# Performance work log

Measured on AMD Instinct MI355X. Metric: run time of the kernel, lower is better.

Reference implementation:

```python
import jax, jax.numpy as jnp
import numpy as np

N_NODES = 8192
N_EDGES = 524288
IN_DIM = 256
HID1 = 128
HID2 = 64


def setup_inputs() -> dict:
    key = jax.random.key(0)
    ks = jax.random.split(key, 10)
    s = 0.05
    x = jax.random.normal(ks[0], (N_NODES, IN_DIM), dtype=jnp.float32)
    edge_index = jax.random.randint(ks[1], (2, N_EDGES), 0, N_NODES, dtype=jnp.int64)
    W1 = jax.random.normal(ks[2], (IN_DIM, HID1), dtype=jnp.float32) * s
    b1 = jnp.zeros((HID1,), dtype=jnp.float32)
    W2 = jax.random.normal(ks[3], (IN_DIM, HID1), dtype=jnp.float32) * s
    b2 = jnp.zeros((HID1,), dtype=jnp.float32)
    Wmu = jax.random.normal(ks[4], (2 * HID1, HID2), dtype=jnp.float32) * s
    bmu = jnp.zeros((HID2,), dtype=jnp.float32)
    Wlv = jax.random.normal(ks[5], (2 * HID1, HID2), dtype=jnp.float32) * s
    blv = jnp.zeros((HID2,), dtype=jnp.float32)
    return {"x": x, "edge_index": edge_index, "W1": W1, "b1": b1,
            "W2": W2, "b2": b2, "Wmu": Wmu, "bmu": bmu, "Wlv": Wlv, "blv": blv}


def _gcn(x, W, b, row, col, norm, n):
    # linear transform, edge-indexed gather, degree-normalized scale, scatter-add
    h = x @ W                                   # [N, out]
    msg = h[col] * norm[:, None]                # [E+N, out]
    agg = jax.ops.segment_sum(msg, row, num_segments=n)
    return agg + b


def reference(x, edge_index, W1, b1, W2, b2, Wmu, bmu, Wlv, blv):
    n = x.shape[0]
    loop = jnp.arange(n, dtype=edge_index.dtype)
    row = jnp.concatenate([edge_index[0], loop])   # add self-loops (GCNConv default)
    col = jnp.concatenate([edge_index[1], loop])
    deg = jax.ops.segment_sum(jnp.ones_like(row, dtype=x.dtype), row, num_segments=n)
    dinv = jnp.where(deg > 0, jax.lax.rsqrt(deg), 0.0)
    norm = dinv[row] * dinv[col]                   # symmetric D^-1/2 A_hat D^-1/2

    h1 = _gcn(x, W1, b1, row, col, norm, n)
    h2 = _gcn(x, W2, b2, row, col, norm, n)
    hc = jnp.concatenate([h1, h2], axis=1)         # [N, 2*HID1]
    mu = _gcn(hc, Wmu, bmu, row, col, norm, n)
    logvar = _gcn(hc, Wlv, blv, row, col, norm, n)
    z = mu                                         # eval-mode reparametrize -> mu
    adj = jax.nn.sigmoid(z @ z.T)                  # InnerProductDecoder.forward_all
    return adj, mu, logvar
```

## Files before the change

### kernel.cpp

```cpp
#include <hip/hip_runtime.h>
#include <hip/hip_bf16.h>

#define N_NODES 8192
#define N_EDGES 524288
#define TOT_EDGES (N_EDGES + N_NODES)
#define IN_DIM 256
#define HID1 128
#define HID2 64
#define DC 128
#define CAP 192
#define FILL_BLK 520

typedef __attribute__((ext_vector_type(8))) short bf16x8;
typedef __attribute__((ext_vector_type(4))) float f32x4;
typedef __attribute__((ext_vector_type(4))) int   i32x4;
typedef __attribute__((ext_vector_type(4))) unsigned short u16x4;

__device__ __forceinline__ float b2f(unsigned short u){
    unsigned int v = ((unsigned int)u) << 16;
    float f; __builtin_memcpy(&f, &v, 4); return f;
}
__device__ __forceinline__ unsigned short f2b(float f){
    __hip_bfloat16 h = __float2bfloat16(f);
    return *(unsigned short*)&h;
}


__global__ __launch_bounds__(256) void k_pre(const float* __restrict__ x, unsigned short* __restrict__ xbf,
                                             const float* __restrict__ W1, const float* __restrict__ W2,
                                             const float* __restrict__ Wmu, const float* __restrict__ Wlv,
                                             const float* __restrict__ b1, const float* __restrict__ b2,
                                             unsigned short* __restrict__ WcT, float* __restrict__ cvec,
                                             float* __restrict__ zbase){
    int b = blockIdx.x, t = threadIdx.x;
    if (b < 2048){
        int g = (b*256 + t)*4;
        f32x4 v = *(const f32x4*)(x + g);
        u16x4 o;
        #pragma unroll
        for (int j=0;j<4;j++) o[j] = f2b(v[j]);
        *(u16x4*)(xbf + g) = o;
    } else if (b < 2176){
        int r = (b - 2048)*2 + (t >> 7);
        int j = t & 127;
        const float* Wsel = (j < 64) ? Wmu : Wlv;
        int jj = j & 63;
        float acc = 0.f;
        for (int k=0;k<HID1;k++){
            acc += W1[r*HID1+k] * Wsel[k*HID2+jj] + W2[r*HID1+k] * Wsel[(HID1+k)*HID2+jj];
        }
        WcT[(size_t)j*IN_DIM + r] = f2b(acc);
        if (r == 0){
            float c = 0.f;
            for (int k=0;k<HID1;k++){
                c += b1[k]*Wsel[k*HID2+jj] + b2[k]*Wsel[(HID1+k)*HID2+jj];
            }
            cvec[j] = c;
        }
    } else {
        ((f32x4*)zbase)[(b-2176)*256 + t] = (f32x4){0.f,0.f,0.f,0.f};
    }
}


__global__ __launch_bounds__(256) void k_fill_gemm(const int* __restrict__ ei, int* __restrict__ fillc,
                                                   unsigned short* __restrict__ slots,
                                                   const unsigned short* __restrict__ xbf,
                                                   const unsigned short* __restrict__ WcT,
                                                   unsigned short* __restrict__ Ubf){
    int b = blockIdx.x, t = threadIdx.x;
    if (b < FILL_BLK){
        int e4 = (b*256 + t)*4;
        if (e4 >= TOT_EDGES) return;
        if (e4 < N_EDGES){
            i32x4 rr = *(const i32x4*)(ei + e4);
            i32x4 cc = *(const i32x4*)(ei + N_EDGES + e4);
            #pragma unroll
            for (int j=0;j<4;j++){
                int s = atomicAdd(&fillc[rr[j]], 1);
                if (s < CAP) slots[(size_t)rr[j]*CAP + s] = (unsigned short)cc[j];
            }
        } else {
            #pragma unroll
            for (int j=0;j<4;j++){
                int r = e4 - N_EDGES + j;
                int s = atomicAdd(&fillc[r], 1);
                if (s < CAP) slots[(size_t)r*CAP + s] = (unsigned short)r;
            }
        }
    } else {
        int l  = t & 63;
        int w  = t >> 6;
        int Ibase = (b - FILL_BLK)*32;
        int Jbase = w*32;
        int lr = l & 15;
        int kg = l >> 4;
        f32x4 acc[2][2];
        #pragma unroll
        for (int mt=0;mt<2;mt++)
            #pragma unroll
            for (int nt=0;nt<2;nt++) acc[mt][nt] = (f32x4){0.f,0.f,0.f,0.f};
        #pragma unroll
        for (int kc=0; kc<IN_DIM/32; kc++){
            bf16x8 a[2], bb[2];
            #pragma unroll
            for (int mt=0;mt<2;mt++)
                a[mt] = *(const bf16x8*)(xbf + (size_t)(Ibase+mt*16+lr)*IN_DIM + kc*32 + kg*8);
            #pragma unroll
            for (int nt=0;nt<2;nt++)
                bb[nt] = *(const bf16x8*)(WcT + (size_t)(Jbase+nt*16+lr)*IN_DIM + kc*32 + kg*8);
            #pragma unroll
            for (int mt=0;mt<2;mt++)
                #pragma unroll
                for (int nt=0;nt<2;nt++)
                    acc[mt][nt] = __builtin_amdgcn_mfma_f32_16x16x32_bf16(a[mt], bb[nt], acc[mt][nt], 0, 0, 0);
        }
        #pragma unroll
        for (int mt=0;mt<2;mt++)
            #pragma unroll
            for (int r=0;r<4;r++){
                int grow = Ibase + mt*16 + kg*4 + r;
                #pragma unroll
                for (int nt=0;nt<2;nt++)
                    Ubf[(size_t)grow*DC + Jbase + nt*16 + lr] = f2b(acc[mt][nt][r]);
            }
    }
}


__global__ __launch_bounds__(256) void k_spmm(const unsigned short* __restrict__ IN,
                                              const unsigned short* __restrict__ slots,
                                              const int* __restrict__ fillc,
                                              unsigned short* __restrict__ OUT){
    int tid = threadIdx.x;
    int i = blockIdx.x*4 + (tid >> 6);
    int l  = tid & 15;
    int eg = (tid >> 4) & 3;
    int deg = min(fillc[i], CAP);
    const unsigned short* sl = slots + (size_t)i*CAP;
    float acc[8] = {0.f,0.f,0.f,0.f,0.f,0.f,0.f,0.f};
    for (int e = eg; e < deg; e += 4){
        int c = sl[e];
        float wgt = rsqrtf((float)fillc[c]);
        bf16x8 v = *(const bf16x8*)(IN + (size_t)c*DC + l*8);
        #pragma unroll
        for (int j=0;j<8;j++) acc[j] += wgt * b2f((unsigned short)v[j]);
    }
    #pragma unroll
    for (int j=0;j<8;j++){
        acc[j] += __shfl_xor(acc[j], 16);
        acc[j] += __shfl_xor(acc[j], 32);
    }
    if (eg == 0){
        float di = rsqrtf((float)fillc[i]);
        bf16x8 o;
        #pragma unroll
        for (int j=0;j<8;j++) o[j] = (short)f2b(di*acc[j]);
        *(bf16x8*)(OUT + (size_t)i*DC + l*8) = o;
    }
}


__global__ __launch_bounds__(256) void k_spmm_out(const unsigned short* __restrict__ T,
                                                  const unsigned short* __restrict__ slots,
                                                  const int* __restrict__ fillc,
                                                  const float* __restrict__ cvec,
                                                  const float* __restrict__ bmu, const float* __restrict__ blv,
                                                  float* __restrict__ outMu, float* __restrict__ outLv,
                                                  unsigned short* __restrict__ muBf){
    int tid = threadIdx.x;
    int i = blockIdx.x*4 + (tid >> 6);
    int l  = tid & 15;
    int eg = (tid >> 4) & 3;
    int deg = min(fillc[i], CAP);
    const unsigned short* sl = slots + (size_t)i*CAP;
    float acc[8] = {0.f,0.f,0.f,0.f,0.f,0.f,0.f,0.f};
    float wsum = 0.f;
    for (int e = eg; e < deg; e += 4){
        int c = sl[e];
        float wgt = rsqrtf((float)fillc[c]);
        wsum += wgt;
        bf16x8 v = *(const bf16x8*)(T + (size_t)c*DC + l*8);
        #pragma unroll
        for (int j=0;j<8;j++) acc[j] += wgt * b2f((unsigned short)v[j]);
    }
    #pragma unroll
    for (int j=0;j<8;j++){
        acc[j] += __shfl_xor(acc[j], 16);
        acc[j] += __shfl_xor(acc[j], 32);
    }
    wsum += __shfl_xor(wsum, 16);
    wsum += __shfl_xor(wsum, 32);
    if (eg == 0){
        float di = rsqrtf((float)fillc[i]);
        float sv = di * wsum;
        float val[8];
        #pragma unroll
        for (int j=0;j<8;j++) val[j] = di*acc[j] + sv*cvec[l*8+j];
        if (l < 8){
            f32x4 v0, v1; bf16x8 o;
            #pragma unroll
            for (int j=0;j<8;j++){
                float vv = val[j] + bmu[l*8+j];
                if (j<4) v0[j] = vv; else v1[j-4] = vv;
                o[j] = (short)f2b(vv);
            }
            *(f32x4*)(outMu + (size_t)i*HID2 + l*8)     = v0;
            *(f32x4*)(outMu + (size_t)i*HID2 + l*8 + 4) = v1;
            *(bf16x8*)(muBf + (size_t)i*HID2 + l*8)     = o;
        } else {
            int d = (l-8)*8;
            f32x4 v0, v1;
            #pragma unroll
            for (int j=0;j<8;j++){
                float vv = val[j] + blv[d+j];
                if (j<4) v0[j] = vv; else v1[j-4] = vv;
            }
            *(f32x4*)(outLv + (size_t)i*HID2 + d)     = v0;
            *(f32x4*)(outLv + (size_t)i*HID2 + d + 4) = v1;
        }
    }
}


__global__ __launch_bounds__(256) void k_adj(const unsigned short* __restrict__ mu, float* __restrict__ adj){
    int t  = threadIdx.x;
    int l  = t & 63;
    int w  = t >> 6;
    int wr = w >> 1, wc = w & 1;
    int Ibase = blockIdx.y*128 + wr*64;
    int Jbase0 = blockIdx.x*128;
    int Jbase = Jbase0 + wc*64;
    int lr = l & 15;
    int kg = l >> 4;

    bf16x8 afr[4][2], bfr[4][2];
    #pragma unroll
    for (int mt=0; mt<4; mt++){
        const unsigned short* p = mu + (size_t)(Ibase + mt*16 + lr)*HID2 + kg*8;
        afr[mt][0] = *(const bf16x8*)(p);
        afr[mt][1] = *(const bf16x8*)(p + 32);
    }
    #pragma unroll
    for (int nt=0; nt<4; nt++){
        const unsigned short* p = mu + (size_t)(Jbase + nt*16 + lr)*HID2 + kg*8;
        bfr[nt][0] = *(const bf16x8*)(p);
        bfr[nt][1] = *(const bf16x8*)(p + 32);
    }

    f32x4 acc[4][4];
    #pragma unroll
    for (int mt=0; mt<4; mt++)
        #pragma unroll
        for (int nt=0; nt<4; nt++)
            acc[mt][nt] = (f32x4){0.f,0.f,0.f,0.f};

    #pragma unroll
    for (int kc=0; kc<2; kc++)
        #pragma unroll
        for (int mt=0; mt<4; mt++)
            #pragma unroll
            for (int nt=0; nt<4; nt++)
                acc[mt][nt] = __builtin_amdgcn_mfma_f32_16x16x32_bf16(afr[mt][kc], bfr[nt][kc], acc[mt][nt], 0, 0, 0);

    __shared__ float tile[64][132];
    int rowBlockBase = blockIdx.y*128;
    #pragma unroll
    for (int p=0; p<2; p++){
        if (wr == p){
            #pragma unroll
            for (int mt=0; mt<4; mt++)
                #pragma unroll
                for (int r=0; r<4; r++){
                    int row_local = mt*16 + kg*4 + r;
                    #pragma unroll
                    for (int nt=0; nt<4; nt++)
                        tile[row_local][wc*64 + nt*16 + lr] = acc[mt][nt][r];
                }
        }
        __syncthreads();
        #pragma unroll
        for (int rep=0; rep<8; rep++){
            int row_r = rep*8 + (t >> 5);
            int col   = (t & 31)*4;
            f32x4 v = *(const f32x4*)&tile[row_r][col];
            f32x4 o;
            #pragma unroll
            for (int j=0;j<4;j++)
                o[j] = __builtin_amdgcn_rcpf(1.f + __expf(-v[j]));
            int grow = rowBlockBase + p*64 + row_r;
            *(f32x4*)(adj + (size_t)grow*N_NODES + Jbase0 + col) = o;
        }
        __syncthreads();
    }
}


extern "C" void kernel_launch(void* const* d_in, const int* in_sizes, int n_in,
                              void* d_out, int out_size, void* d_ws, size_t ws_size,
                              hipStream_t stream){
    const float* x   = (const float*)d_in[0];
    const int*   ei  = (const int*)  d_in[1];
    const float* W1  = (const float*)d_in[2];
    const float* b1  = (const float*)d_in[3];
    const float* W2  = (const float*)d_in[4];
    const float* b2  = (const float*)d_in[5];
    const float* Wmu = (const float*)d_in[6];
    const float* bmu = (const float*)d_in[7];
    const float* Wlv = (const float*)d_in[8];
    const float* blv = (const float*)d_in[9];

    char* ws = (char*)d_ws;
    int*   fillc  = (int*)  (ws + 0);
    unsigned short* WcT = (unsigned short*)(ws + 32768);
    float* cvec   = (float*)(ws + 98304);
    unsigned short* muBf = (unsigned short*)(ws + 98816);
    unsigned short* xbf  = (unsigned short*)(ws + 1147392);

    float* adj   = (float*)d_out;
    float* outMu = adj + (size_t)N_NODES*N_NODES;
    float* outLv = outMu + (size_t)N_NODES*HID2;

    unsigned short* Ubf   = (unsigned short*)adj;
    unsigned short* Tbf   = (unsigned short*)((char*)adj + 16*1024*1024);
    unsigned short* slots = (unsigned short*)((char*)adj + 32*1024*1024);

    k_pre      <<<2184, 256, 0, stream>>>(x, xbf, W1, W2, Wmu, Wlv, b1, b2, WcT, cvec, (float*)ws);
    k_fill_gemm<<<FILL_BLK + 256, 256, 0, stream>>>(ei, fillc, slots, xbf, WcT, Ubf);
    k_spmm     <<<N_NODES/4, 256, 0, stream>>>(Ubf, slots, fillc, Tbf);
    k_spmm_out <<<N_NODES/4, 256, 0, stream>>>(Tbf, slots, fillc, cvec, bmu, blv,
                                               outMu, outLv, muBf);
    k_adj      <<<dim3(N_NODES/128, N_NODES/128), 256, 0, stream>>>(muBf, adj);
}
```

Before: 133.0 us.

## Fuse x bf16 conversion into GEMM and use per-wave adj epilogue

Drops the separate pass that converts x to bf16 in k_pre; the GEMM now loads fp32 x directly and converts in registers, which removes an 8 MB read plus a 4 MB write and makes k_pre much smaller. The adj epilogue switches from a block-wide shared tile with __syncthreads to a per-wave 16x64 LDS staging buffer that uses only waitcnt, so no block barriers are needed and less shared memory is used. In exchange, each GEMM block now reads twice as many bytes of x, and the adj row stores become narrower (256B per row segment rather than 512B).

```diff
diff --git a/kernel.cpp b/kernel.cpp
--- a/kernel.cpp
+++ b/kernel.cpp
@@ -26,22 +26,16 @@
 }
 
 
-__global__ __launch_bounds__(256) void k_pre(const float* __restrict__ x, unsigned short* __restrict__ xbf,
-                                             const float* __restrict__ W1, const float* __restrict__ W2,
+__global__ __launch_bounds__(256) void k_pre(const float* __restrict__ W1, const float* __restrict__ W2,
                                              const float* __restrict__ Wmu, const float* __restrict__ Wlv,
                                              const float* __restrict__ b1, const float* __restrict__ b2,
                                              unsigned short* __restrict__ WcT, float* __restrict__ cvec,
                                              float* __restrict__ zbase){
     int b = blockIdx.x, t = threadIdx.x;
-    if (b < 2048){
-        int g = (b*256 + t)*4;
-        f32x4 v = *(const f32x4*)(x + g);
-        u16x4 o;
-        #pragma unroll
-        for (int j=0;j<4;j++) o[j] = f2b(v[j]);
-        *(u16x4*)(xbf + g) = o;
-    } else if (b < 2176){
-        int r = (b - 2048)*2 + (t >> 7);
+    if (b < 8){
+        ((f32x4*)zbase)[b*256 + t] = (f32x4){0.f,0.f,0.f,0.f};
+    } else {
+        int r = (b - 8)*2 + (t >> 7);
         int j = t & 127;
         const float* Wsel = (j < 64) ? Wmu : Wlv;
         int jj = j & 63;
@@ -57,15 +51,13 @@
             }
             cvec[j] = c;
         }
-    } else {
-        ((f32x4*)zbase)[(b-2176)*256 + t] = (f32x4){0.f,0.f,0.f,0.f};
     }
 }
 
 
 __global__ __launch_bounds__(256) void k_fill_gemm(const int* __restrict__ ei, int* __restrict__ fillc,
                                                    unsigned short* __restrict__ slots,
-                                                   const unsigned short* __restrict__ xbf,
+                                                   const float* __restrict__ x,
                                                    const unsigned short* __restrict__ WcT,
                                                    unsigned short* __restrict__ Ubf){
     int b = blockIdx.x, t = threadIdx.x;
@@ -104,8 +96,16 @@
         for (int kc=0; kc<IN_DIM/32; kc++){
             bf16x8 a[2], bb[2];
             #pragma unroll
-            for (int mt=0;mt<2;mt++)
-                a[mt] = *(const bf16x8*)(xbf + (size_t)(Ibase+mt*16+lr)*IN_DIM + kc*32 + kg*8);
+            for (int mt=0;mt<2;mt++){
+                const float* xr = x + (size_t)(Ibase+mt*16+lr)*IN_DIM + kc*32 + kg*8;
+                f32x4 v0 = *(const f32x4*)xr;
+                f32x4 v1 = *(const f32x4*)(xr + 4);
+                #pragma unroll
+                for (int j=0;j<4;j++){
+                    a[mt][j]   = (short)f2b(v0[j]);
+                    a[mt][4+j] = (short)f2b(v1[j]);
+                }
+            }
             #pragma unroll
             for (int nt=0;nt<2;nt++)
                 bb[nt] = *(const bf16x8*)(WcT + (size_t)(Jbase+nt*16+lr)*IN_DIM + kc*32 + kg*8);
@@ -229,8 +229,7 @@
     int w  = t >> 6;
     int wr = w >> 1, wc = w & 1;
     int Ibase = blockIdx.y*128 + wr*64;
-    int Jbase0 = blockIdx.x*128;
-    int Jbase = Jbase0 + wc*64;
+    int Jbase = blockIdx.x*128 + wc*64;
     int lr = l & 15;
     int kg = l >> 4;
 
@@ -263,35 +262,29 @@
             for (int nt=0; nt<4; nt++)
                 acc[mt][nt] = __builtin_amdgcn_mfma_f32_16x16x32_bf16(afr[mt][kc], bfr[nt][kc], acc[mt][nt], 0, 0, 0);
 
-    __shared__ float tile[64][132];
-    int rowBlockBase = blockIdx.y*128;
-    #pragma unroll
-    for (int p=0; p<2; p++){
-        if (wr == p){
-            #pragma unroll
-            for (int mt=0; mt<4; mt++)
-                #pragma unroll
-                for (int r=0; r<4; r++){
-                    int row_local = mt*16 + kg*4 + r;
-                    #pragma unroll
-                    for (int nt=0; nt<4; nt++)
-                        tile[row_local][wc*64 + nt*16 + lr] = acc[mt][nt][r];
-                }
-        }
-        __syncthreads();
-        #pragma unroll
-        for (int rep=0; rep<8; rep++){
-            int row_r = rep*8 + (t >> 5);
-            int col   = (t & 31)*4;
-            f32x4 v = *(const f32x4*)&tile[row_r][col];
+    __shared__ float wt[4][16][68];
+    float* myt = &wt[w][0][0];
+    #pragma unroll
+    for (int mt=0; mt<4; mt++){
+        asm volatile("s_waitcnt lgkmcnt(0)" ::: "memory");
+        #pragma unroll
+        for (int nt=0; nt<4; nt++)
+            #pragma unroll
+            for (int r=0; r<4; r++)
+                myt[(kg*4+r)*68 + nt*16 + lr] = acc[mt][nt][r];
+        asm volatile("s_waitcnt lgkmcnt(0)" ::: "memory");
+        __builtin_amdgcn_sched_barrier(0);
+        #pragma unroll
+        for (int p=0; p<4; p++){
+            int row = p*4 + (l >> 4);
+            int col = (l & 15)*4;
+            f32x4 v = *(const f32x4*)&myt[row*68 + col];
             f32x4 o;
             #pragma unroll
             for (int j=0;j<4;j++)
                 o[j] = __builtin_amdgcn_rcpf(1.f + __expf(-v[j]));
-            int grow = rowBlockBase + p*64 + row_r;
-            *(f32x4*)(adj + (size_t)grow*N_NODES + Jbase0 + col) = o;
-        }
-        __syncthreads();
+            *(f32x4*)(adj + (size_t)(Ibase + mt*16 + row)*N_NODES + Jbase + col) = o;
+        }
     }
 }
 
@@ -315,7 +308,6 @@
     unsigned short* WcT = (unsigned short*)(ws + 32768);
     float* cvec   = (float*)(ws + 98304);
     unsigned short* muBf = (unsigned short*)(ws + 98816);
-    unsigned short* xbf  = (unsigned short*)(ws + 1147392);
 
     float* adj   = (float*)d_out;
     float* outMu = adj + (size_t)N_NODES*N_NODES;
@@ -325,8 +317,8 @@
     unsigned short* Tbf   = (unsigned short*)((char*)adj + 16*1024*1024);
     unsigned short* slots = (unsigned short*)((char*)adj + 32*1024*1024);
 
-    k_pre      <<<2184, 256, 0, stream>>>(x, xbf, W1, W2, Wmu, Wlv, b1, b2, WcT, cvec, (float*)ws);
-    k_fill_gemm<<<FILL_BLK + 256, 256, 0, stream>>>(ei, fillc, slots, xbf, WcT, Ubf);
+    k_pre      <<<136, 256, 0, stream>>>(W1, W2, Wmu, Wlv, b1, b2, WcT, cvec, (float*)ws);
+    k_fill_gemm<<<FILL_BLK + 256, 256, 0, stream>>>(ei, fillc, slots, x, WcT, Ubf);
     k_spmm     <<<N_NODES/4, 256, 0, stream>>>(Ubf, slots, fillc, Tbf);
     k_spmm_out <<<N_NODES/4, 256, 0, stream>>>(Tbf, slots, fillc, cvec, bmu, blv,
                                                outMu, outLv, muBf);
```

Result: faster. 128.5 us (-3.4%).
